# Kernel optimization log

Hardware: AMD Instinct MI355X
Metric: run time of the kernel (lower is better)

Reference implementation:

```python
import jax, jax.numpy as jnp
import numpy as np

I, H, V, T, B = 108, 1024, 108, 180, 512


def setup_inputs() -> dict:
    key = jax.random.key(0)
    ks = jax.random.split(key, 13)
    sc = 1.0 / np.sqrt(H).astype(np.float32)
    rn = lambda k, shape: (jax.random.normal(k, shape, jnp.float32) * sc)
    return {
        "x": jax.random.normal(ks[0], (T, B, I), jnp.float32),
        # LSTMCell 1 (input -> hidden)
        "W_ih1": rn(ks[1], (4 * H, I)), "W_hh1": rn(ks[2], (4 * H, H)),
        "b_ih1": rn(ks[3], (4 * H,)), "b_hh1": rn(ks[4], (4 * H,)),
        # mid Linear (hidden -> hidden)
        "W_mid": rn(ks[5], (H, H)), "b_mid": rn(ks[6], (H,)),
        # LSTMCell 2 (hidden -> hidden)
        "W_ih2": rn(ks[7], (4 * H, H)), "W_hh2": rn(ks[8], (4 * H, H)),
        "b_ih2": rn(ks[9], (4 * H,)), "b_hh2": rn(ks[10], (4 * H,)),
        # final Linear (hidden -> output)
        "W_fin": rn(ks[11], (V, H)), "b_fin": rn(ks[12], (V,)),
    }


def _lstm_cell(xt, h, c, W_ih, W_hh, b_ih, b_hh):
    # PyTorch LSTMCell gate order: input, forget, cell(g), output
    gates = xt @ W_ih.T + b_ih + h @ W_hh.T + b_hh  # [B, 4H]
    i, f, g, o = jnp.split(gates, 4, axis=-1)
    c_new = jax.nn.sigmoid(f) * c + jax.nn.sigmoid(i) * jnp.tanh(g)
    h_new = jax.nn.sigmoid(o) * jnp.tanh(c_new)
    return h_new, c_new


def reference(x, W_ih1, W_hh1, b_ih1, b_hh1, W_mid, b_mid,
              W_ih2, W_hh2, b_ih2, b_hh2, W_fin, b_fin):
    Bsz = x.shape[1]
    Hsz = W_hh1.shape[1]

    def step(carry, xt):
        h1, c1, h2, c2 = carry
        h1, c1 = _lstm_cell(xt, h1, c1, W_ih1, W_hh1, b_ih1, b_hh1)
        # NOTE: original feeds the CELL state (state1) into mid, not hidden1
        m = c1 @ W_mid.T + b_mid
        h2, c2 = _lstm_cell(m, h2, c2, W_ih2, W_hh2, b_ih2, b_hh2)
        # final also reads the cell state (state2); dropout is identity (eval)
        out = jax.nn.log_softmax(c2 @ W_fin.T + b_fin, axis=-1)
        return (h1, c1, h2, c2), out

    init = tuple(jnp.zeros((Bsz, Hsz), x.dtype) for _ in range(4))
    (h1, c1, h2, c2), outs = jax.lax.scan(step, init, x)  # outs: [T, B, V]
    return outs
```

## Files before the change

### kernel.cpp

```cpp
#include <hip/hip_runtime.h>
#include <stdint.h>


typedef unsigned short u16;
typedef __attribute__((ext_vector_type(2))) float f32x2;
typedef __attribute__((ext_vector_type(4))) float f32x4;
typedef __attribute__((ext_vector_type(8))) short bf16x8;
typedef unsigned long long u64;

#define HDIM 1024
#define BSZ  512
#define TSTEPS 180
#define IIN  108
#define VOUT 108
#define NBLK 256

#define AGENT __HIP_MEMORY_SCOPE_AGENT
#define RLX   __ATOMIC_RELAXED

__device__ __forceinline__ u16 f2bf(float x) {
  union { float f; unsigned u; } v; v.f = x;
  unsigned r = (v.u + 0x7fffu + ((v.u >> 16) & 1u)) >> 16;
  return (u16)r;
}
// ... 1 lines not shown
  union { unsigned u; float f; } v; v.u = (b & 0xffffu) << 16; return v.f;
}
__device__ __forceinline__ float sigm(float x) { return 1.f / (1.f + __expf(-x)); }
__device__ __forceinline__ float tanh_(float x) {
  float a = fabsf(x), t = __expf(-2.f * a);
  float r = (1.f - t) / (1.f + t);
  return x < 0.f ? -r : r;
}
__device__ __forceinline__ int permrow(int n) { return ((n & 1023) << 2) | (n >> 10); }

template <int AUX>
__device__ __forceinline__ void load16_lds(const void* g, void* l) {
  __builtin_amdgcn_global_load_lds(
      (const __attribute__((address_space(1))) unsigned int*)g,
      (__attribute__((address_space(3))) unsigned int*)l, 16, 0, AUX);
}

__device__ __forceinline__ void st32(void* p, unsigned v) {
  __hip_atomic_store((unsigned*)p, v, RLX, AGENT);
}
__device__ __forceinline__ void st64(void* p, u64 v) {
  __hip_atomic_store((u64*)p, v, RLX, AGENT);
}
__device__ __forceinline__ u64 ld64(const void* p) {
  return __hip_atomic_load((u64*)p, RLX, AGENT);
}

__device__ __forceinline__ void grid_sync(unsigned* bar, int grp) {
  __syncthreads();
  if (threadIdx.x == 0) {
    unsigned* gen  = bar;
    unsigned* root = bar + 32;
    unsigned* gcnt = bar + 64 + grp * 32;
    unsigned g = __hip_atomic_load(gen, RLX, AGENT);
    asm volatile("s_waitcnt vmcnt(0)" ::: "memory");
    unsigned a = __hip_atomic_fetch_add(gcnt, 1u, RLX, AGENT);
    if (a == 31u) {
      __hip_atomic_store(gcnt, 0u, RLX, AGENT);
      asm volatile("s_waitcnt vmcnt(0)" ::: "memory");
      unsigned c = __hip_atomic_fetch_add(root, 1u, RLX, AGENT);
      if (c == 7u) {
        __hip_atomic_store(root, 0u, RLX, AGENT);
        asm volatile("s_waitcnt vmcnt(0)" ::: "memory");
        __hip_atomic_store(gen, g + 1u, RLX, AGENT);
      }
    }
    while (__hip_atomic_load(gen, RLX, AGENT) == g)
      __builtin_amdgcn_s_sleep(2);
  }
  __syncthreads();
}

template <int AUXA>
__device__ __forceinline__ void stage128(const u16* A, const u16* B, int K,
                                         int k0, int m0, int n0,
                                         char* smem, int buf, int wave, int lane) {
  u16* As = (u16*)(smem + buf * 32768);
  u16* Bs = (u16*)(smem + buf * 32768 + 16384);
#pragma unroll
  for (int i = 0; i < 4; ++i) {
    int c = (wave * 4 + i) * 64 + lane;
    int row = c >> 3, lc = (c & 7) ^ (row & 7);
    const u16* g = A + (size_t)(m0 + row) * K + k0 + (lc << 3);
    load16_lds<AUXA>(g, As + c * 8);
  }
#pragma unroll
  for (int i = 0; i < 4; ++i) {
    int c = (wave * 4 + i) * 64 + lane;
    int row = c >> 3, lc = (c & 7) ^ (row & 7);
    const u16* g = B + (size_t)(n0 + row) * K + k0 + (lc << 3);
    load16_lds<0>(g, Bs + c * 8);
  }
}

__device__ __forceinline__ void compute128(f32x4 acc[4][4], char* smem, int buf,
                                           int wm, int wn, int l16, int quad) {
  const bf16x8* Av = (const bf16x8*)(smem + buf * 32768);
  const bf16x8* Bv = (const bf16x8*)(smem + buf * 32768 + 16384);
  const int sw = l16 & 7;
#pragma unroll
  for (int kk = 0; kk < 2; ++kk) {
    const int pc = (kk * 4 + quad) ^ sw;
    bf16x8 a[4], b[4];
#pragma unroll
    for (int mt = 0; mt < 4; ++mt)
      a[mt] = Av[(wm * 64 + mt * 16 + l16) * 8 + pc];
#pragma unroll
    for (int nt = 0; nt < 4; ++nt)
      b[nt] = Bv[(wn * 64 + nt * 16 + l16) * 8 + pc];
#pragma unroll
    for (int mt = 0; mt < 4; ++mt)
#pragma unroll
      for (int nt = 0; nt < 4; ++nt)
        acc[mt][nt] = __builtin_amdgcn_mfma_f32_16x16x32_bf16(
            a[mt], b[nt], acc[mt][nt], 0, 0, 0);
  }
}

template <bool HAS0>
__device__ __forceinline__ void gemm128(f32x4 acc[4][4],
    const u16* A0, const u16* B0, int K0,
    const u16* A1, const u16* B1, int K1,
    int m0, int n0, char* smem) {
  const int tid = threadIdx.x;
  const int lane = tid & 63, wave = tid >> 6;
  const int quad = lane >> 4, l16 = lane & 15;
  const int wm = wave >> 1, wn = wave & 1;

#pragma unroll
  for (int mt = 0; mt < 4; ++mt)
#pragma unroll
    for (int nt = 0; nt < 4; ++nt) {
      f32x4 z = {0.f, 0.f, 0.f, 0.f};
      acc[mt][nt] = z;
    }

  const int n0i = HAS0 ? (K0 >> 6) : 0;
  const int nIter = n0i + (K1 >> 6);

  auto do_stage = [&](int ix) {
    if (HAS0 && ix < n0i)
      stage128<0>(A0, B0, K0, ix * 64, m0, n0, smem, ix & 3, wave, lane);
    else
      stage128<0x11>(A1, B1, K1, (ix - n0i) * 64, m0, n0, smem, ix & 3, wave, lane);
  };

  do_stage(0);
  if (nIter > 1) do_stage(1);
  if (nIter > 2) do_stage(2);

  for (int it = 0; it < nIter; ++it) {
    if (it + 3 < nIter) do_stage(it + 3);
    const int rem = nIter - 1 - it;
    if (rem >= 3)      asm volatile("s_waitcnt vmcnt(24)" ::: "memory");
    else if (rem == 2) asm volatile("s_waitcnt vmcnt(16)" ::: "memory");
    else if (rem == 1) asm volatile("s_waitcnt vmcnt(8)"  ::: "memory");
    else               asm volatile("s_waitcnt vmcnt(0)"  ::: "memory");
    __builtin_amdgcn_s_barrier();
    asm volatile("" ::: "memory");
    compute128(acc, smem, it & 3, wm, wn, l16, quad);
    asm volatile("" ::: "memory");
    __builtin_amdgcn_s_barrier();
  }
}

__device__ __forceinline__ void stage_pb(const u16* A, const u16* B, int k0,
                                         int m0, int n0, char* smem, int buf,
                                         int wave, int lane) {
  u16* As = (u16*)(smem + buf * 24576);
  u16* Bs = (u16*)(smem + buf * 24576 + 16384);
#pragma unroll
  for (int i = 0; i < 4; ++i) {
    int c = (wave * 4 + i) * 64 + lane;
    int row = c >> 3, lc = (c & 7) ^ (row & 7);
    load16_lds<0x11>(A + (size_t)(m0 + row) * 1024 + k0 + (lc << 3), As + c * 8);
  }
#pragma unroll
  for (int i = 0; i < 2; ++i) {
    int c = (wave * 2 + i) * 64 + lane;
    int row = c >> 3, lc = (c & 7) ^ (row & 7);
    load16_lds<0>(B + (size_t)(n0 + row) * 1024 + k0 + (lc << 3), Bs + c * 8);
  }
}

__device__ __forceinline__ void compute_pb(f32x4 acc[4][2], char* smem, int buf,
                                           int wm, int wn, int l16, int quad) {
  const bf16x8* Av = (const bf16x8*)(smem + buf * 24576);
  const bf16x8* Bv = (const bf16x8*)(smem + buf * 24576 + 16384);
  const int sw = l16 & 7;
#pragma unroll
  for (int kk = 0; kk < 2; ++kk) {
    const int pc = (kk * 4 + quad) ^ sw;
    bf16x8 a[4], b[2];
#pragma unroll
    for (int mt = 0; mt < 4; ++mt)
      a[mt] = Av[(wm * 64 + mt * 16 + l16) * 8 + pc];
#pragma unroll
    for (int nt = 0; nt < 2; ++nt)
      b[nt] = Bv[(wn * 32 + nt * 16 + l16) * 8 + pc];
#pragma unroll
    for (int mt = 0; mt < 4; ++mt)
#pragma unroll
      for (int nt = 0; nt < 2; ++nt)
        acc[mt][nt] = __builtin_amdgcn_mfma_f32_16x16x32_bf16(
            a[mt], b[nt], acc[mt][nt], 0, 0, 0);
  }
}

__global__ __launch_bounds__(256, 1) void lstm_persistent(
    const u16* __restrict__ Xbf, const u16* __restrict__ W1a,
    const u16* __restrict__ Whh1b, const float* __restrict__ b1s,
    float* __restrict__ C1f, u16* __restrict__ C1b,
    const u16* __restrict__ Whh2b, const float* __restrict__ b2s,
    u16* __restrict__ U2, const u16* __restrict__ Wcombb,
    float* __restrict__ C2f, u16* __restrict__ C2seq,
    u16* __restrict__ H1x, u16* __restrict__ H1y,
    u16* __restrict__ H2x, u16* __restrict__ H2y,
    unsigned* __restrict__ bar)
{
  __shared__ __align__(16) char smem[131072];
  const int tid = threadIdx.x;
  const int lane = tid & 63, wave = tid >> 6;
  const int quad = lane >> 4, l16 = lane & 15;
  const int wm = wave >> 1, wn = wave & 1;
  const int b = blockIdx.x;
  const int grp = b & 7;

  for (int t = 0; t < TSTEPS; ++t) {
    const int p = t & 1;
    const u16* H1in = p ? H1y : H1x;  u16* H1o = p ? H1x : H1y;
    const u16* H2in = p ? H2y : H2x;  u16* H2o = p ? H2x : H2y;
    const u16* Xt = Xbf + (size_t)t * BSZ * 128;

    if (b < 128) {
      f32x4 acc[4][4];
      const int m0 = (b >> 5) * 128, n0 = (b & 31) * 128;
      gemm128<true>(acc, Xt, W1a, 128, H1in, Whh1b, 1024, m0, n0, smem);

      float* gl = (float*)smem;
      const int jbase = (b & 31) * 32;
#pragma unroll
      for (int h = 0; h < 2; ++h) {
        __syncthreads();
        if (wm == h) {
#pragma unroll
          for (int nt = 0; nt < 4; ++nt) {
            int col = wn * 64 + nt * 16 + l16;
#pragma unroll
            for (int mt = 0; mt < 4; ++mt) {
              int rowb = mt * 16 + quad * 4;
#pragma unroll
              for (int r = 0; r < 4; ++r)
                gl[(rowb + r) * 132 + col] = acc[mt][nt][r];
            }
          }
        }
        __syncthreads();
#pragma unroll
        for (int itr = 0; itr < 4; ++itr) {
          int idx = itr * 256 + tid;
          int mr = idx >> 4, jp = idx & 15;
          const float* gp = gl + mr * 132 + jp * 8;
          f32x4 ga = *(const f32x4*)gp;
          f32x4 gb = *(const f32x4*)(gp + 4);
          const float* bp = b1s + jbase * 4 + jp * 8;
          ga += *(const f32x4*)bp;
          gb += *(const f32x4*)(bp + 4);
          size_t off = (size_t)(m0 + h * 64 + mr) * HDIM + jbase + jp * 2;
          f32x2 cp = *(const f32x2*)(C1f + off);
          float c0 = sigm(ga[1]) * cp[0] + sigm(ga[0]) * tanh_(ga[2]);
          float c1 = sigm(gb[1]) * cp[1] + sigm(gb[0]) * tanh_(gb[2]);
          float h0 = sigm(ga[3]) * tanh_(c0);
          float h1 = sigm(gb[3]) * tanh_(c1);
          f32x2 cn = {c0, c1};
          *(f32x2*)(C1f + off) = cn;
          st32(H1o + off, (unsigned)f2bf(h0) | ((unsigned)f2bf(h1) << 16));
          st32(C1b + off, (unsigned)f2bf(c0) | ((unsigned)f2bf(c1) << 16));
        }
      }
    } else {
      f32x4 acc[4][4];
      const int bb = b - 128;
      const int m0 = (bb >> 5) * 128, n0 = (bb & 31) * 128;
      gemm128<false>(acc, nullptr, nullptr, 0, H2in, Whh2b, 1024, m0, n0, smem);
#pragma unroll
      for (int nt = 0; nt < 4; ++nt) {
        int col = n0 + wn * 64 + nt * 16 + l16;
        float bias = b2s[col];
#pragma unroll
        for (int mt = 0; mt < 4; ++mt) {
          int row = m0 + wm * 64 + mt * 16 + quad * 4;
#pragma unroll
          for (int r = 0; r < 4; ++r) {
            float v = acc[mt][nt][r] + bias;
            float w = __shfl_xor(v, 1);
            if (!(lane & 1))
              st32(U2 + (size_t)(row + r) * 4096 + col,
                   (unsigned)f2bf(v) | ((unsigned)f2bf(w) << 16));
          }
        }
      }
    }
    grid_sync(bar, grp);

    {
      f32x4 acc[4][2];
#pragma unroll
      for (int mt = 0; mt < 4; ++mt)
#pragma unroll
        for (int nt = 0; nt < 2; ++nt) {
          f32x4 z = {0.f, 0.f, 0.f, 0.f};
          acc[mt][nt] = z;
        }
      const int m0 = (b >> 6) * 128;
      const int n0 = (b & 63) * 64;
      const int jbase = (b & 63) * 16;

      stage_pb(C1b, Wcombb, 0,   m0, n0, smem, 0, wave, lane);
      stage_pb(C1b, Wcombb, 64,  m0, n0, smem, 1, wave, lane);
      stage_pb(C1b, Wcombb, 128, m0, n0, smem, 2, wave, lane);
      for (int it = 0; it < 16; ++it) {
        if (it + 3 < 16)
          stage_pb(C1b, Wcombb, (it + 3) * 64, m0, n0, smem, (it + 3) & 3, wave, lane);
        const int rem = 15 - it;
        if (rem >= 3)      asm volatile("s_waitcnt vmcnt(18)" ::: "memory");
        else if (rem == 2) asm volatile("s_waitcnt vmcnt(12)" ::: "memory");
        else if (rem == 1) asm volatile("s_waitcnt vmcnt(6)"  ::: "memory");
        else               asm volatile("s_waitcnt vmcnt(0)"  ::: "memory");
        __builtin_amdgcn_s_barrier();
        asm volatile("" ::: "memory");
        compute_pb(acc, smem, it & 3, wm, wn, l16, quad);
        asm volatile("" ::: "memory");
        __builtin_amdgcn_s_barrier();
      }

      float* gl = (float*)smem;
      __syncthreads();
#pragma unroll
      for (int nt = 0; nt < 2; ++nt) {
        int col = wn * 32 + nt * 16 + l16;
#pragma unroll
        for (int mt = 0; mt < 4; ++mt) {
          int rowb = wm * 64 + mt * 16 + quad * 4;
#pragma unroll
          for (int r = 0; r < 4; ++r)
            gl[(rowb + r) * 68 + col] = acc[mt][nt][r];
        }
      }
      __syncthreads();
      u16* C2dst = C2seq + (size_t)t * BSZ * HDIM;
#pragma unroll
      for (int itr = 0; itr < 4; ++itr) {
        int idx = itr * 256 + tid;
        int mr = idx >> 3, jp = idx & 7;
        int grow = m0 + mr;
        const float* gp = gl + mr * 68 + jp * 8;
        f32x4 ga = *(const f32x4*)gp;
        f32x4 gb = *(const f32x4*)(gp + 4);
        const u16* u2p = U2 + (size_t)grow * 4096 + (jbase + jp * 2) * 4;
        u64 ua = ld64(u2p);
        u64 ub = ld64(u2p + 4);
        ga[0] += bf2f((unsigned)ua);        ga[1] += bf2f((unsigned)(ua >> 16));
        ga[2] += bf2f((unsigned)(ua >> 32)); ga[3] += bf2f((unsigned)(ua >> 48));
        gb[0] += bf2f((unsigned)ub);        gb[1] += bf2f((unsigned)(ub >> 16));
        gb[2] += bf2f((unsigned)(ub >> 32)); gb[3] += bf2f((unsigned)(ub >> 48));
        size_t off = (size_t)grow * HDIM + jbase + jp * 2;
        union { u64 u; float f[2]; } cv;
        cv.u = ld64(C2f + off);
        float c0 = sigm(ga[1]) * cv.f[0] + sigm(ga[0]) * tanh_(ga[2]);
        float c1 = sigm(gb[1]) * cv.f[1] + sigm(gb[0]) * tanh_(gb[2]);
        float h0 = sigm(ga[3]) * tanh_(c0);
        float h1 = sigm(gb[3]) * tanh_(c1);
        cv.f[0] = c0; cv.f[1] = c1;
        st64(C2f + off, cv.u);
        st32(H2o + off, (unsigned)f2bf(h0) | ((unsigned)f2bf(h1) << 16));
        st32(C2dst + off, (unsigned)f2bf(c0) | ((unsigned)f2bf(c1) << 16));
      }
    }
    grid_sync(bar, grp);
  }
}

__global__ __launch_bounds__(256, 1) void k1_fused(
    const u16* __restrict__ Xt, const u16* __restrict__ W1a,
    const u16* __restrict__ H1in, const u16* __restrict__ Whh1,
    const float* __restrict__ b1s, float* __restrict__ c1State,
    u16* __restrict__ H1out, u16* __restrict__ C1out,
    const u16* __restrict__ H2in, const u16* __restrict__ Whh2,
    const float* __restrict__ b2s, u16* __restrict__ U2)
{
  __shared__ __align__(16) char smem[131072];
  const int tid = threadIdx.x;
  const int lane = tid & 63, wave = tid >> 6;
  const int quad = lane >> 4, l16 = lane & 15;
  const int wm = wave >> 1, wn = wave & 1;
  const int b = blockIdx.x;
  f32x4 acc[4][4];

  if (b < 128) {
    const int m0 = (b >> 5) * 128, n0 = (b & 31) * 128;
    gemm128<true>(acc, Xt, W1a, 128, H1in, Whh1, 1024, m0, n0, smem);

    float* gl = (float*)smem;
    const int jbase = (b & 31) * 32;
#pragma unroll
    for (int h = 0; h < 2; ++h) {
      __syncthreads();
      if (wm == h) {
#pragma unroll
        for (int nt = 0; nt < 4; ++nt) {
          int col = wn * 64 + nt * 16 + l16;
#pragma unroll
          for (int mt = 0; mt < 4; ++mt) {
            int rowb = mt * 16 + quad * 4;
#pragma unroll
            for (int r = 0; r < 4; ++r)
              gl[(rowb + r) * 132 + col] = acc[mt][nt][r];
          }
        }
      }
      __syncthreads();
#pragma unroll
      for (int itr = 0; itr < 8; ++itr) {
        int idx = itr * 256 + tid;
        int mr = idx >> 5, jl = idx & 31;
        f32x4 g4 = *(const f32x4*)(gl + mr * 132 + jl * 4);
        f32x4 b4 = *(const f32x4*)(b1s + jbase * 4 + jl * 4);
        g4 += b4;
        float ii = sigm(g4[0]), ff = sigm(g4[1]);
        float gg = tanh_(g4[2]), oo = sigm(g4[3]);
        size_t off = (size_t)(m0 + h * 64 + mr) * HDIM + jbase + jl;
        float cp = c1State[off];
        float cn = ff * cp + ii * gg;
        float hh = oo * tanh_(cn);
        c1State[off] = cn;
// ... 294 lines not shown
  const size_t SZ_C2S = (size_t)TSTEPS * BSZ * HDIM * 2;

  char* base = (char*)d_ws;
  size_t off = 0;
  auto alloc = [&](size_t b) { char* p = base + off; off += (b + 255) & ~(size_t)255; return p; };

  u16*   Xbf    = (u16*)alloc(SZ_XBF);
  u16*   W1a    = (u16*)alloc(SZ_W1A);
  u16*   Whh1b  = (u16*)alloc(SZ_W1K);
  u16*   Wcombb = (u16*)alloc(SZ_W1K);
  u16*   Whh2b  = (u16*)alloc(SZ_W1K);
  u16*   Wih2b  = (u16*)alloc(SZ_W1K);
  u16*   WmidT  = (u16*)alloc(SZ_WMT);
  u16*   Wfinb  = (u16*)alloc(SZ_WFB);
  float* b1s    = (float*)alloc(SZ_BSM);
  float* b2s    = (float*)alloc(SZ_BSM);
  u16*   H1p[2]; H1p[0] = (u16*)alloc(SZ_HB); H1p[1] = (u16*)alloc(SZ_HB);
  u16*   H2p[2]; H2p[0] = (u16*)alloc(SZ_HB); H2p[1] = (u16*)alloc(SZ_HB);
  float* C1f    = (float*)alloc(SZ_CF);
  float* C2f    = (float*)alloc(SZ_CF);
  u16*   C1b    = (u16*)alloc(SZ_HB);
  u16*   C2b    = (u16*)alloc(SZ_HB);
  u16*   U2     = (u16*)alloc(SZ_U2);
  unsigned* barp = (unsigned*)alloc(2048);
  u16*   C2seq  = (u16*)(base + off);
  bool batched  = (off + SZ_C2S) <= ws_size;

  size_t zbytes = 4 * SZ_HB + 2 * SZ_CF;
  hipMemsetAsync((void*)H1p[0], 0, zbytes, stream);
  hipMemsetAsync((void*)barp, 0, 2048, stream);

  k_build_w1a<<<2048, 256, 0, stream>>>(Wih1, W1a);
  k_conv_perm1024<<<16384, 256, 0, stream>>>(Whh1, Whh1b);
  k_conv_perm1024<<<16384, 256, 0, stream>>>(Whh2, Whh2b);
  k_conv<<<16384, 256, 0, stream>>>(Wih2, Wih2b);
  k_transpose1024<<<4096, 256, 0, stream>>>(Wmid, WmidT);
  k_build_wfin<<<512, 256, 0, stream>>>(Wfin, Wfinb);
  k_build_xpad<<<46080, 256, 0, stream>>>(x, Xbf);
  k_b1sum<<<16, 256, 0, stream>>>(bih1, bhh1, b1s);
  k_b2sum<<<1024, 256, 0, stream>>>(Wih2, bmid, bih2, bhh2, b2s);
  wcomb_gemm<<<dim3(8, 64), 256, 0, stream>>>(Wih2b, WmidT, Wcombb);

  bool usedPersistent = false;
  if (batched) {
    u16* H1x = H1p[0]; u16* H1y = H1p[1];
    u16* H2x = H2p[0]; u16* H2y = H2p[1];
    void* kargs[] = {
        (void*)&Xbf, (void*)&W1a, (void*)&Whh1b, (void*)&b1s,
        (void*)&C1f, (void*)&C1b, (void*)&Whh2b, (void*)&b2s,
        (void*)&U2, (void*)&Wcombb, (void*)&C2f, (void*)&C2seq,
        (void*)&H1x, (void*)&H1y, (void*)&H2x, (void*)&H2y,
        (void*)&barp};
    hipError_t ce = hipLaunchCooperativeKernel(
        (const void*)lstm_persistent, dim3(NBLK), dim3(256), kargs, 0, stream);
    usedPersistent = (ce == hipSuccess);
    if (!usedPersistent) (void)hipGetLastError();
  }

  if (usedPersistent) {
    final_logsoftmax<<<dim3(1, (TSTEPS * BSZ) / 64), 256, 0, stream>>>(
        C2seq, Wfinb, bfin, (float*)d_out);
  } else {
    for (int t = 0; t < TSTEPS; ++t) {
      int p = t & 1;
      k1_fused<<<256, 256, 0, stream>>>(
          Xbf + (size_t)t * BSZ * 128, W1a, H1p[p], Whh1b, b1s, C1f,
          H1p[p ^ 1], C1b, H2p[p], Whh2b, b2s, U2);
      u16* c2dst = batched ? (C2seq + (size_t)t * BSZ * HDIM) : C2b;
      k2_cell2<<<128, 256, 0, stream>>>(C1b, Wcombb, U2, C2f, H2p[p ^ 1], c2dst);
      if (!batched)
        final_logsoftmax<<<dim3(1, 8), 256, 0, stream>>>(
            C2b, Wfinb, bfin, (float*)d_out + (size_t)t * BSZ * VOUT);
    }
    if (batched)
      final_logsoftmax<<<dim3(1, (TSTEPS * BSZ) / 64), 256, 0, stream>>>(
          C2seq, Wfinb, bfin, (float*)d_out);
  }
}
```

Before: 6.854 ms.

## Use 8 waves per block in persistent LSTM kernel

After: 5.753 ms, median of 2. 1.19x faster.

```diff
diff --git a/kernel.cpp b/kernel.cpp
--- a/kernel.cpp
+++ b/kernel.cpp
@@ -77,65 +77,63 @@
 }
 
 template <int AUXA>
-__device__ __forceinline__ void stage128(const u16* A, const u16* B, int K,
-                                         int k0, int m0, int n0,
-                                         char* smem, int buf, int wave, int lane) {
+__device__ __forceinline__ void stage128_8w(const u16* A, const u16* B, int K,
+                                            int k0, int m0, int n0,
+                                            char* smem, int buf, int wave, int lane) {
   u16* As = (u16*)(smem + buf * 32768);
   u16* Bs = (u16*)(smem + buf * 32768 + 16384);
 #pragma unroll
-  for (int i = 0; i < 4; ++i) {
-    int c = (wave * 4 + i) * 64 + lane;
+  for (int i = 0; i < 2; ++i) {
+    int c = (wave * 2 + i) * 64 + lane;
     int row = c >> 3, lc = (c & 7) ^ (row & 7);
-    const u16* g = A + (size_t)(m0 + row) * K + k0 + (lc << 3);
-    load16_lds<AUXA>(g, As + c * 8);
-  }
-#pragma unroll
-  for (int i = 0; i < 4; ++i) {
-    int c = (wave * 4 + i) * 64 + lane;
+    load16_lds<AUXA>(A + (size_t)(m0 + row) * K + k0 + (lc << 3), As + c * 8);
+  }
+#pragma unroll
+  for (int i = 0; i < 2; ++i) {
+    int c = (wave * 2 + i) * 64 + lane;
     int row = c >> 3, lc = (c & 7) ^ (row & 7);
-    const u16* g = B + (size_t)(n0 + row) * K + k0 + (lc << 3);
-    load16_lds<0>(g, Bs + c * 8);
-  }
-}
-
-__device__ __forceinline__ void compute128(f32x4 acc[4][4], char* smem, int buf,
-                                           int wm, int wn, int l16, int quad) {
+    load16_lds<0>(B + (size_t)(n0 + row) * K + k0 + (lc << 3), Bs + c * 8);
+  }
+}
+
+__device__ __forceinline__ void compute128_8w(f32x4 acc[4][2], char* smem, int buf,
+                                              int wm, int wn, int l16, int quad) {
   const bf16x8* Av = (const bf16x8*)(smem + buf * 32768);
   const bf16x8* Bv = (const bf16x8*)(smem + buf * 32768 + 16384);
   const int sw = l16 & 7;
 #pragma unroll
   for (int kk = 0; kk < 2; ++kk) {
     const int pc = (kk * 4 + quad) ^ sw;
-    bf16x8 a[4], b[4];
+    bf16x8 a[4], b[2];
 #pragma unroll
     for (int mt = 0; mt < 4; ++mt)
       a[mt] = Av[(wm * 64 + mt * 16 + l16) * 8 + pc];
 #pragma unroll
-    for (int nt = 0; nt < 4; ++nt)
-      b[nt] = Bv[(wn * 64 + nt * 16 + l16) * 8 + pc];
+    for (int nt = 0; nt < 2; ++nt)
+      b[nt] = Bv[(wn * 32 + nt * 16 + l16) * 8 + pc];
 #pragma unroll
     for (int mt = 0; mt < 4; ++mt)
 #pragma unroll
-      for (int nt = 0; nt < 4; ++nt)
+      for (int nt = 0; nt < 2; ++nt)
         acc[mt][nt] = __builtin_amdgcn_mfma_f32_16x16x32_bf16(
             a[mt], b[nt], acc[mt][nt], 0, 0, 0);
   }
 }
 
 template <bool HAS0>
-__device__ __forceinline__ void gemm128(f32x4 acc[4][4],
+__device__ __forceinline__ void gemm128_8w(f32x4 acc[4][2],
     const u16* A0, const u16* B0, int K0,
     const u16* A1, const u16* B1, int K1,
     int m0, int n0, char* smem) {
   const int tid = threadIdx.x;
   const int lane = tid & 63, wave = tid >> 6;
   const int quad = lane >> 4, l16 = lane & 15;
-  const int wm = wave >> 1, wn = wave & 1;
+  const int wm = wave >> 2, wn = wave & 3;
 
 #pragma unroll
   for (int mt = 0; mt < 4; ++mt)
 #pragma unroll
-    for (int nt = 0; nt < 4; ++nt) {
+    for (int nt = 0; nt < 2; ++nt) {
       f32x4 z = {0.f, 0.f, 0.f, 0.f};
       acc[mt][nt] = z;
     }
@@ -145,9 +143,9 @@
 
   auto do_stage = [&](int ix) {
     if (HAS0 && ix < n0i)
-      stage128<0>(A0, B0, K0, ix * 64, m0, n0, smem, ix & 3, wave, lane);
+      stage128_8w<0>(A0, B0, K0, ix * 64, m0, n0, smem, ix & 3, wave, lane);
     else
-      stage128<0x11>(A1, B1, K1, (ix - n0i) * 64, m0, n0, smem, ix & 3, wave, lane);
+      stage128_8w<0x11>(A1, B1, K1, (ix - n0i) * 64, m0, n0, smem, ix & 3, wave, lane);
   };
 
   do_stage(0);
@@ -157,62 +155,56 @@
   for (int it = 0; it < nIter; ++it) {
     if (it + 3 < nIter) do_stage(it + 3);
     const int rem = nIter - 1 - it;
-    if (rem >= 3)      asm volatile("s_waitcnt vmcnt(24)" ::: "memory");
-    else if (rem == 2) asm volatile("s_waitcnt vmcnt(16)" ::: "memory");
-    else if (rem == 1) asm volatile("s_waitcnt vmcnt(8)"  ::: "memory");
+    if (rem >= 3)      asm volatile("s_waitcnt vmcnt(12)" ::: "memory");
+    else if (rem == 2) asm volatile("s_waitcnt vmcnt(8)"  ::: "memory");
+    else if (rem == 1) asm volatile("s_waitcnt vmcnt(4)"  ::: "memory");
     else               asm volatile("s_waitcnt vmcnt(0)"  ::: "memory");
     __builtin_amdgcn_s_barrier();
     asm volatile("" ::: "memory");
-    compute128(acc, smem, it & 3, wm, wn, l16, quad);
+    compute128_8w(acc, smem, it & 3, wm, wn, l16, quad);
     asm volatile("" ::: "memory");
     __builtin_amdgcn_s_barrier();
   }
 }
 
-__device__ __forceinline__ void stage_pb(const u16* A, const u16* B, int k0,
-                                         int m0, int n0, char* smem, int buf,
-                                         int wave, int lane) {
+__device__ __forceinline__ void stage_pb_8w(const u16* A, const u16* B, int k0,
+                                            int m0, int n0, char* smem, int buf,
+                                            int wave, int lane) {
   u16* As = (u16*)(smem + buf * 24576);
   u16* Bs = (u16*)(smem + buf * 24576 + 16384);
-#pragma unroll
-  for (int i = 0; i < 4; ++i) {
-    int c = (wave * 4 + i) * 64 + lane;
-    int row = c >> 3, lc = (c & 7) ^ (row & 7);
-    load16_lds<0x11>(A + (size_t)(m0 + row) * 1024 + k0 + (lc << 3), As + c * 8);
-  }
 #pragma unroll
   for (int i = 0; i < 2; ++i) {
     int c = (wave * 2 + i) * 64 + lane;
     int row = c >> 3, lc = (c & 7) ^ (row & 7);
+    load16_lds<0x11>(A + (size_t)(m0 + row) * 1024 + k0 + (lc << 3), As + c * 8);
+  }
+  {
+    int c = wave * 64 + lane;
+    int row = c >> 3, lc = (c & 7) ^ (row & 7);
     load16_lds<0>(B + (size_t)(n0 + row) * 1024 + k0 + (lc << 3), Bs + c * 8);
   }
 }
 
-__device__ __forceinline__ void compute_pb(f32x4 acc[4][2], char* smem, int buf,
-                                           int wm, int wn, int l16, int quad) {
+__device__ __forceinline__ void compute_pb_8w(f32x4 acc[4], char* smem, int buf,
+                                              int wm, int wn, int l16, int quad) {
   const bf16x8* Av = (const bf16x8*)(smem + buf * 24576);
   const bf16x8* Bv = (const bf16x8*)(smem + buf * 24576 + 16384);
   const int sw = l16 & 7;
 #pragma unroll
   for (int kk = 0; kk < 2; ++kk) {
     const int pc = (kk * 4 + quad) ^ sw;
-    bf16x8 a[4], b[2];
+    bf16x8 a[4], b;
 #pragma unroll
     for (int mt = 0; mt < 4; ++mt)
       a[mt] = Av[(wm * 64 + mt * 16 + l16) * 8 + pc];
-#pragma unroll
-    for (int nt = 0; nt < 2; ++nt)
-      b[nt] = Bv[(wn * 32 + nt * 16 + l16) * 8 + pc];
+    b = Bv[(wn * 16 + l16) * 8 + pc];
 #pragma unroll
     for (int mt = 0; mt < 4; ++mt)
-#pragma unroll
-      for (int nt = 0; nt < 2; ++nt)
-        acc[mt][nt] = __builtin_amdgcn_mfma_f32_16x16x32_bf16(
-            a[mt], b[nt], acc[mt][nt], 0, 0, 0);
-  }
-}
-
-__global__ __launch_bounds__(256, 1) void lstm_persistent(
+      acc[mt] = __builtin_amdgcn_mfma_f32_16x16x32_bf16(a[mt], b, acc[mt], 0, 0, 0);
+  }
+}
+
+__global__ __launch_bounds__(512, 1) void lstm_persistent(
     const u16* __restrict__ Xbf, const u16* __restrict__ W1a,
     const u16* __restrict__ Whh1b, const float* __restrict__ b1s,
     float* __restrict__ C1f, u16* __restrict__ C1b,
@@ -227,7 +219,7 @@
   const int tid = threadIdx.x;
   const int lane = tid & 63, wave = tid >> 6;
   const int quad = lane >> 4, l16 = lane & 15;
-  const int wm = wave >> 1, wn = wave & 1;
+  const int wm = wave >> 2, wn = wave & 3;
   const int b = blockIdx.x;
   const int grp = b & 7;
 
@@ -238,9 +230,9 @@
     const u16* Xt = Xbf + (size_t)t * BSZ * 128;
 
     if (b < 128) {
-      f32x4 acc[4][4];
+      f32x4 acc[4][2];
       const int m0 = (b >> 5) * 128, n0 = (b & 31) * 128;
-      gemm128<true>(acc, Xt, W1a, 128, H1in, Whh1b, 1024, m0, n0, smem);
+      gemm128_8w<true>(acc, Xt, W1a, 128, H1in, Whh1b, 1024, m0, n0, smem);
 
       float* gl = (float*)smem;
       const int jbase = (b & 31) * 32;
@@ -249,8 +241,8 @@
         __syncthreads();
         if (wm == h) {
 #pragma unroll
-          for (int nt = 0; nt < 4; ++nt) {
-            int col = wn * 64 + nt * 16 + l16;
+          for (int nt = 0; nt < 2; ++nt) {
+            int col = wn * 32 + nt * 16 + l16;
 #pragma unroll
             for (int mt = 0; mt < 4; ++mt) {
               int rowb = mt * 16 + quad * 4;
@@ -262,8 +254,8 @@
         }
         __syncthreads();
 #pragma unroll
-        for (int itr = 0; itr < 4; ++itr) {
-          int idx = itr * 256 + tid;
+        for (int itr = 0; itr < 2; ++itr) {
+          int idx = itr * 512 + tid;
           int mr = idx >> 4, jp = idx & 15;
           const float* gp = gl + mr * 132 + jp * 8;
           f32x4 ga = *(const f32x4*)gp;
@@ -284,13 +276,13 @@
         }
       }
     } else {
-      f32x4 acc[4][4];
+      f32x4 acc[4][2];
       const int bb = b - 128;
       const int m0 = (bb >> 5) * 128, n0 = (bb & 31) * 128;
-      gemm128<false>(acc, nullptr, nullptr, 0, H2in, Whh2b, 1024, m0, n0, smem);
-#pragma unroll
-      for (int nt = 0; nt < 4; ++nt) {
-        int col = n0 + wn * 64 + nt * 16 + l16;
+      gemm128_8w<false>(acc, nullptr, nullptr, 0, H2in, Whh2b, 1024, m0, n0, smem);
+#pragma unroll
+      for (int nt = 0; nt < 2; ++nt) {
+        int col = n0 + wn * 32 + nt * 16 + l16;
         float bias = b2s[col];
 #pragma unroll
         for (int mt = 0; mt < 4; ++mt) {
@@ -309,54 +301,51 @@
     grid_sync(bar, grp);
 
     {
-      f32x4 acc[4][2];
-#pragma unroll
-      for (int mt = 0; mt < 4; ++mt)
-#pragma unroll
-        for (int nt = 0; nt < 2; ++nt) {
-          f32x4 z = {0.f, 0.f, 0.f, 0.f};
-          acc[mt][nt] = z;
-        }
+      f32x4 acc[4];
+#pragma unroll
+      for (int mt = 0; mt < 4; ++mt) {
+        f32x4 z = {0.f, 0.f, 0.f, 0.f};
+        acc[mt] = z;
+      }
       const int m0 = (b >> 6) * 128;
       const int n0 = (b & 63) * 64;
       const int jbase = (b & 63) * 16;
 
-      stage_pb(C1b, Wcombb, 0,   m0, n0, smem, 0, wave, lane);
-      stage_pb(C1b, Wcombb, 64,  m0, n0, smem, 1, wave, lane);
-      stage_pb(C1b, Wcombb, 128, m0, n0, smem, 2, wave, lane);
+      stage_pb_8w(C1b, Wcombb, 0,   m0, n0, smem, 0, wave, lane);
+      stage_pb_8w(C1b, Wcombb, 64,  m0, n0, smem, 1, wave, lane);
+      stage_pb_8w(C1b, Wcombb, 128, m0, n0, smem, 2, wave, lane);
       for (int it = 0; it < 16; ++it) {
         if (it + 3 < 16)
-          stage_pb(C1b, Wcombb, (it + 3) * 64, m0, n0, smem, (it + 3) & 3, wave, lane);
+          stage_pb_8w(C1b, Wcombb, (it + 3) * 64, m0, n0, smem, (it + 3) & 3, wave, lane);
         const int rem = 15 - it;
-        if (rem >= 3)      asm volatile("s_waitcnt vmcnt(18)" ::: "memory");
-        else if (rem == 2) asm volatile("s_waitcnt vmcnt(12)" ::: "memory");
-        else if (rem == 1) asm volatile("s_waitcnt vmcnt(6)"  ::: "memory");
-        else               asm volatile("s_waitcnt vmcnt(0)"  ::: "memory");
+        if (rem >= 3)      asm volatile("s_waitcnt vmcnt(9)" ::: "memory");
+        else if (rem == 2) asm volatile("s_waitcnt vmcnt(6)" ::: "memory");
+        else if (rem == 1) asm volatile("s_waitcnt vmcnt(3)" ::: "memory");
+        else               asm volatile("s_waitcnt vmcnt(0)" ::: "memory");
         __builtin_amdgcn_s_barrier();
         asm volatile("" ::: "memory");
-        compute_pb(acc, smem, it & 3, wm, wn, l16, quad);
+        compute_pb_8w(acc, smem, it & 3, wm, wn, l16, quad);
         asm volatile("" ::: "memory");
         __builtin_amdgcn_s_barrier();
       }
 
       float* gl = (float*)smem;
       __syncthreads();
-#pragma unroll
-      for (int nt = 0; nt < 2; ++nt) {
-        int col = wn * 32 + nt * 16 + l16;
+      {
+        int col = wn * 16 + l16;
 #pragma unroll
         for (int mt = 0; mt < 4; ++mt) {
           int rowb = wm * 64 + mt * 16 + quad * 4;
 #pragma unroll
           for (int r = 0; r < 4; ++r)
-            gl[(rowb + r) * 68 + col] = acc[mt][nt][r];
+            gl[(rowb + r) * 68 + col] = acc[mt][r];
         }
       }
       __syncthreads();
       u16* C2dst = C2seq + (size_t)t * BSZ * HDIM;
 #pragma unroll
-      for (int itr = 0; itr < 4; ++itr) {
-        int idx = itr * 256 + tid;
+      for (int itr = 0; itr < 2; ++itr) {
+        int idx = itr * 512 + tid;
         int mr = idx >> 3, jp = idx & 7;
         int grow = m0 + mr;
         const float* gp = gl + mr * 68 + jp * 8;
@@ -386,6 +375,97 @@
   }
 }
 
+template <int AUXA>
+__device__ __forceinline__ void stage128(const u16* A, const u16* B, int K,
+                                         int k0, int m0, int n0,
+                                         char* smem, int buf, int wave, int lane) {
+  u16* As = (u16*)(smem + buf * 32768);
+  u16* Bs = (u16*)(smem + buf * 32768 + 16384);
+#pragma unroll
+  for (int i = 0; i < 4; ++i) {
+    int c = (wave * 4 + i) * 64 + lane;
+    int row = c >> 3, lc = (c & 7) ^ (row & 7);
+    load16_lds<AUXA>(A + (size_t)(m0 + row) * K + k0 + (lc << 3), As + c * 8);
+  }
+#pragma unroll
+  for (int i = 0; i < 4; ++i) {
+    int c = (wave * 4 + i) * 64 + lane;
+    int row = c >> 3, lc = (c & 7) ^ (row & 7);
+    load16_lds<0>(B + (size_t)(n0 + row) * K + k0 + (lc << 3), Bs + c * 8);
+  }
+}
+
+__device__ __forceinline__ void compute128(f32x4 acc[4][4], char* smem, int buf,
+                                           int wm, int wn, int l16, int quad) {
+  const bf16x8* Av = (const bf16x8*)(smem + buf * 32768);
+  const bf16x8* Bv = (const bf16x8*)(smem + buf * 32768 + 16384);
+  const int sw = l16 & 7;
+#pragma unroll
+  for (int kk = 0; kk < 2; ++kk) {
+    const int pc = (kk * 4 + quad) ^ sw;
+    bf16x8 a[4], b[4];
+#pragma unroll
+    for (int mt = 0; mt < 4; ++mt)
+      a[mt] = Av[(wm * 64 + mt * 16 + l16) * 8 + pc];
+#pragma unroll
+    for (int nt = 0; nt < 4; ++nt)
+      b[nt] = Bv[(wn * 64 + nt * 16 + l16) * 8 + pc];
+#pragma unroll
+    for (int mt = 0; mt < 4; ++mt)
+#pragma unroll
+      for (int nt = 0; nt < 4; ++nt)
+        acc[mt][nt] = __builtin_amdgcn_mfma_f32_16x16x32_bf16(
+            a[mt], b[nt], acc[mt][nt], 0, 0, 0);
+  }
+}
+
+template <bool HAS0>
+__device__ __forceinline__ void gemm128(f32x4 acc[4][4],
+    const u16* A0, const u16* B0, int K0,
+    const u16* A1, const u16* B1, int K1,
+    int m0, int n0, char* smem) {
+  const int tid = threadIdx.x;
+  const int lane = tid & 63, wave = tid >> 6;
+  const int quad = lane >> 4, l16 = lane & 15;
+  const int wm = wave >> 1, wn = wave & 1;
+
+#pragma unroll
+  for (int mt = 0; mt < 4; ++mt)
+#pragma unroll
+    for (int nt = 0; nt < 4; ++nt) {
+      f32x4 z = {0.f, 0.f, 0.f, 0.f};
+      acc[mt][nt] = z;
+    }
+
+  const int n0i = HAS0 ? (K0 >> 6) : 0;
+  const int nIter = n0i + (K1 >> 6);
+
+  auto do_stage = [&](int ix) {
+    if (HAS0 && ix < n0i)
+      stage128<0>(A0, B0, K0, ix * 64, m0, n0, smem, ix & 3, wave, lane);
+    else
+      stage128<0x11>(A1, B1, K1, (ix - n0i) * 64, m0, n0, smem, ix & 3, wave, lane);
+  };
+
+  do_stage(0);
+  if (nIter > 1) do_stage(1);
+  if (nIter > 2) do_stage(2);
+
+  for (int it = 0; it < nIter; ++it) {
+    if (it + 3 < nIter) do_stage(it + 3);
+    const int rem = nIter - 1 - it;
+    if (rem >= 3)      asm volatile("s_waitcnt vmcnt(24)" ::: "memory");
+    else if (rem == 2) asm volatile("s_waitcnt vmcnt(16)" ::: "memory");
+    else if (rem == 1) asm volatile("s_waitcnt vmcnt(8)"  ::: "memory");
+    else               asm volatile("s_waitcnt vmcnt(0)"  ::: "memory");
+    __builtin_amdgcn_s_barrier();
+    asm volatile("" ::: "memory");
+    compute128(acc, smem, it & 3, wm, wn, l16, quad);
+    asm volatile("" ::: "memory");
+    __builtin_amdgcn_s_barrier();
+  }
+}
+
 __global__ __launch_bounds__(256, 1) void k1_fused(
     const u16* __restrict__ Xt, const u16* __restrict__ W1a,
     const u16* __restrict__ H1in, const u16* __restrict__ Whh1,
@@ -786,7 +866,7 @@
         (void*)&H1x, (void*)&H1y, (void*)&H2x, (void*)&H2y,
         (void*)&barp};
     hipError_t ce = hipLaunchCooperativeKernel(
-        (const void*)lstm_persistent, dim3(NBLK), dim3(256), kargs, 0, stream);
+        (const void*)lstm_persistent, dim3(NBLK), dim3(512), kargs, 0, stream);
     usedPersistent = (ce == hipSuccess);
     if (!usedPersistent) (void)hipGetLastError();
   }
```

## Use 8 waves per block with split-K across wave pairs in persistent LSTM

Applied to the files above, without the earlier changes.

Measured after the change: 8.697 ms. 26.9% more time.

```diff
diff --git a/kernel.cpp b/kernel.cpp
--- a/kernel.cpp
+++ b/kernel.cpp
@@ -77,42 +77,40 @@
 }
 
 template <int AUXA>
-__device__ __forceinline__ void stage128(const u16* A, const u16* B, int K,
-                                         int k0, int m0, int n0,
-                                         char* smem, int buf, int wave, int lane) {
-  u16* As = (u16*)(smem + buf * 32768);
-  u16* Bs = (u16*)(smem + buf * 32768 + 16384);
+__device__ __forceinline__ void stageA(const u16* A, const u16* B, int lda, int ldb,
+                                       int k0, int m0, int n0,
+                                       char* smem, int buf, int wave, int lane) {
+  u16* As = (u16*)(smem + buf * 65536);
+  u16* Bs = (u16*)(smem + buf * 65536 + 32768);
 #pragma unroll
   for (int i = 0; i < 4; ++i) {
     int c = (wave * 4 + i) * 64 + lane;
-    int row = c >> 3, lc = (c & 7) ^ (row & 7);
-    const u16* g = A + (size_t)(m0 + row) * K + k0 + (lc << 3);
-    load16_lds<AUXA>(g, As + c * 8);
+    int row = c >> 4, lc = (c & 15) ^ (row & 15);
+    load16_lds<AUXA>(A + (size_t)(m0 + row) * lda + k0 + (lc << 3), As + c * 8);
   }
 #pragma unroll
   for (int i = 0; i < 4; ++i) {
     int c = (wave * 4 + i) * 64 + lane;
-    int row = c >> 3, lc = (c & 7) ^ (row & 7);
-    const u16* g = B + (size_t)(n0 + row) * K + k0 + (lc << 3);
-    load16_lds<0>(g, Bs + c * 8);
-  }
-}
-
-__device__ __forceinline__ void compute128(f32x4 acc[4][4], char* smem, int buf,
-                                           int wm, int wn, int l16, int quad) {
-  const bf16x8* Av = (const bf16x8*)(smem + buf * 32768);
-  const bf16x8* Bv = (const bf16x8*)(smem + buf * 32768 + 16384);
-  const int sw = l16 & 7;
-#pragma unroll
-  for (int kk = 0; kk < 2; ++kk) {
-    const int pc = (kk * 4 + quad) ^ sw;
+    int row = c >> 4, lc = (c & 15) ^ (row & 15);
+    load16_lds<0>(B + (size_t)(n0 + row) * ldb + k0 + (lc << 3), Bs + c * 8);
+  }
+}
+
+__device__ __forceinline__ void computeA(f32x4 acc[4][4], char* smem, int buf,
+                                         int qm, int qn, int kh, int l16, int quad) {
+  const bf16x8* Av = (const bf16x8*)(smem + buf * 65536);
+  const bf16x8* Bv = (const bf16x8*)(smem + buf * 65536 + 32768);
+#pragma unroll
+  for (int kk2 = 0; kk2 < 2; ++kk2) {
+    const int lchunk = (kh * 2 + kk2) * 4 + quad;
+    const int pc = lchunk ^ l16;
     bf16x8 a[4], b[4];
 #pragma unroll
     for (int mt = 0; mt < 4; ++mt)
-      a[mt] = Av[(wm * 64 + mt * 16 + l16) * 8 + pc];
+      a[mt] = Av[(qm * 64 + mt * 16 + l16) * 16 + pc];
 #pragma unroll
     for (int nt = 0; nt < 4; ++nt)
-      b[nt] = Bv[(wn * 64 + nt * 16 + l16) * 8 + pc];
+      b[nt] = Bv[(qn * 64 + nt * 16 + l16) * 16 + pc];
 #pragma unroll
     for (int mt = 0; mt < 4; ++mt)
 #pragma unroll
@@ -123,15 +121,11 @@
 }
 
 template <bool HAS0>
-__device__ __forceinline__ void gemm128(f32x4 acc[4][4],
-    const u16* A0, const u16* B0, int K0,
-    const u16* A1, const u16* B1, int K1,
-    int m0, int n0, char* smem) {
-  const int tid = threadIdx.x;
-  const int lane = tid & 63, wave = tid >> 6;
-  const int quad = lane >> 4, l16 = lane & 15;
-  const int wm = wave >> 1, wn = wave & 1;
-
+__device__ __forceinline__ void gemmA(f32x4 acc[4][4],
+    const u16* A0, const u16* B0,
+    const u16* A1, const u16* B1,
+    int m0, int n0, char* smem,
+    int wave, int lane, int qm, int qn, int kh, int l16, int quad) {
 #pragma unroll
   for (int mt = 0; mt < 4; ++mt)
 #pragma unroll
@@ -139,70 +133,66 @@
       f32x4 z = {0.f, 0.f, 0.f, 0.f};
       acc[mt][nt] = z;
     }
-
-  const int n0i = HAS0 ? (K0 >> 6) : 0;
-  const int nIter = n0i + (K1 >> 6);
+  const int n0i = HAS0 ? 1 : 0;
+  const int nIter = n0i + 8;
 
   auto do_stage = [&](int ix) {
-    if (HAS0 && ix < n0i)
-      stage128<0>(A0, B0, K0, ix * 64, m0, n0, smem, ix & 3, wave, lane);
+    if (HAS0 && ix == 0)
+      stageA<0>(A0, B0, 128, 128, 0, m0, n0, smem, ix & 1, wave, lane);
     else
-      stage128<0x11>(A1, B1, K1, (ix - n0i) * 64, m0, n0, smem, ix & 3, wave, lane);
+      stageA<0x11>(A1, B1, 1024, 1024, (ix - n0i) * 128, m0, n0, smem, ix & 1, wave, lane);
   };
 
   do_stage(0);
-  if (nIter > 1) do_stage(1);
-  if (nIter > 2) do_stage(2);
-
   for (int it = 0; it < nIter; ++it) {
-    if (it + 3 < nIter) do_stage(it + 3);
-    const int rem = nIter - 1 - it;
-    if (rem >= 3)      asm volatile("s_waitcnt vmcnt(24)" ::: "memory");
-    else if (rem == 2) asm volatile("s_waitcnt vmcnt(16)" ::: "memory");
-    else if (rem == 1) asm volatile("s_waitcnt vmcnt(8)"  ::: "memory");
-    else               asm volatile("s_waitcnt vmcnt(0)"  ::: "memory");
+    if (it + 1 < nIter) {
+      do_stage(it + 1);
+      asm volatile("s_waitcnt vmcnt(8)" ::: "memory");
+    } else {
+      asm volatile("s_waitcnt vmcnt(0)" ::: "memory");
+    }
     __builtin_amdgcn_s_barrier();
     asm volatile("" ::: "memory");
-    compute128(acc, smem, it & 3, wm, wn, l16, quad);
+    computeA(acc, smem, it & 1, qm, qn, kh, l16, quad);
     asm volatile("" ::: "memory");
     __builtin_amdgcn_s_barrier();
   }
 }
 
-__device__ __forceinline__ void stage_pb(const u16* A, const u16* B, int k0,
-                                         int m0, int n0, char* smem, int buf,
-                                         int wave, int lane) {
-  u16* As = (u16*)(smem + buf * 24576);
-  u16* Bs = (u16*)(smem + buf * 24576 + 16384);
+__device__ __forceinline__ void stageB(const u16* A, const u16* B, int k0,
+                                       int m0, int n0, char* smem, int buf,
+                                       int wave, int lane) {
+  u16* As = (u16*)(smem + buf * 49152);
+  u16* Bs = (u16*)(smem + buf * 49152 + 32768);
 #pragma unroll
   for (int i = 0; i < 4; ++i) {
     int c = (wave * 4 + i) * 64 + lane;
-    int row = c >> 3, lc = (c & 7) ^ (row & 7);
+    int row = c >> 4, lc = (c & 15) ^ (row & 15);
     load16_lds<0x11>(A + (size_t)(m0 + row) * 1024 + k0 + (lc << 3), As + c * 8);
   }
 #pragma unroll
   for (int i = 0; i < 2; ++i) {
     int c = (wave * 2 + i) * 64 + lane;
-    int row = c >> 3, lc = (c & 7) ^ (row & 7);
+    int row = c >> 4, lc = (c & 15) ^ (row & 15);
     load16_lds<0>(B + (size_t)(n0 + row) * 1024 + k0 + (lc << 3), Bs + c * 8);
   }
 }
 
-__device__ __forceinline__ void compute_pb(f32x4 acc[4][2], char* smem, int buf,
-                                           int wm, int wn, int l16, int quad) {
-  const bf16x8* Av = (const bf16x8*)(smem + buf * 24576);
-  const bf16x8* Bv = (const bf16x8*)(smem + buf * 24576 + 16384);
-  const int sw = l16 & 7;
-#pragma unroll
-  for (int kk = 0; kk < 2; ++kk) {
-    const int pc = (kk * 4 + quad) ^ sw;
+__device__ __forceinline__ void computeB(f32x4 acc[4][2], char* smem, int buf,
+                                         int qm, int qn, int kh, int l16, int quad) {
+  const bf16x8* Av = (const bf16x8*)(smem + buf * 49152);
+  const bf16x8* Bv = (const bf16x8*)(smem + buf * 49152 + 32768);
+#pragma unroll
+  for (int kk2 = 0; kk2 < 2; ++kk2) {
+    const int lchunk = (kh * 2 + kk2) * 4 + quad;
+    const int pc = lchunk ^ l16;
     bf16x8 a[4], b[2];
 #pragma unroll
     for (int mt = 0; mt < 4; ++mt)
-      a[mt] = Av[(wm * 64 + mt * 16 + l16) * 8 + pc];
+      a[mt] = Av[(qm * 64 + mt * 16 + l16) * 16 + pc];
 #pragma unroll
     for (int nt = 0; nt < 2; ++nt)
-      b[nt] = Bv[(wn * 32 + nt * 16 + l16) * 8 + pc];
+      b[nt] = Bv[(qn * 32 + nt * 16 + l16) * 16 + pc];
 #pragma unroll
     for (int mt = 0; mt < 4; ++mt)
 #pragma unroll
@@ -212,7 +202,7 @@
   }
 }
 
-__global__ __launch_bounds__(256, 1) void lstm_persistent(
+__global__ __launch_bounds__(512, 1) void lstm_persistent(
     const u16* __restrict__ Xbf, const u16* __restrict__ W1a,
     const u16* __restrict__ Whh1b, const float* __restrict__ b1s,
     float* __restrict__ C1f, u16* __restrict__ C1b,
@@ -227,7 +217,7 @@
   const int tid = threadIdx.x;
   const int lane = tid & 63, wave = tid >> 6;
   const int quad = lane >> 4, l16 = lane & 15;
-  const int wm = wave >> 1, wn = wave & 1;
+  const int qm = wave >> 2, qn = (wave >> 1) & 1, kh = wave & 1;
   const int b = blockIdx.x;
   const int grp = b & 7;
 
@@ -240,17 +230,18 @@
     if (b < 128) {
       f32x4 acc[4][4];
       const int m0 = (b >> 5) * 128, n0 = (b & 31) * 128;
-      gemm128<true>(acc, Xt, W1a, 128, H1in, Whh1b, 1024, m0, n0, smem);
+      gemmA<true>(acc, Xt, W1a, H1in, Whh1b, m0, n0, smem,
+                  wave, lane, qm, qn, kh, l16, quad);
 
       float* gl = (float*)smem;
       const int jbase = (b & 31) * 32;
 #pragma unroll
       for (int h = 0; h < 2; ++h) {
         __syncthreads();
-        if (wm == h) {
+        if (qm == h && kh == 1) {
 #pragma unroll
           for (int nt = 0; nt < 4; ++nt) {
-            int col = wn * 64 + nt * 16 + l16;
+            int col = qn * 64 + nt * 16 + l16;
 #pragma unroll
             for (int mt = 0; mt < 4; ++mt) {
               int rowb = mt * 16 + quad * 4;
@@ -261,9 +252,23 @@
           }
         }
         __syncthreads();
-#pragma unroll
-        for (int itr = 0; itr < 4; ++itr) {
-          int idx = itr * 256 + tid;
+        if (qm == h && kh == 0) {
+#pragma unroll
+          for (int nt = 0; nt < 4; ++nt) {
+            int col = qn * 64 + nt * 16 + l16;
+#pragma unroll
+            for (int mt = 0; mt < 4; ++mt) {
+              int rowb = mt * 16 + quad * 4;
+#pragma unroll
+              for (int r = 0; r < 4; ++r)
+                gl[(rowb + r) * 132 + col] += acc[mt][nt][r];
+            }
+          }
+        }
+        __syncthreads();
+#pragma unroll
+        for (int itr = 0; itr < 2; ++itr) {
+          int idx = itr * 512 + tid;
           int mr = idx >> 4, jp = idx & 15;
           const float* gp = gl + mr * 132 + jp * 8;
           f32x4 ga = *(const f32x4*)gp;
@@ -287,23 +292,47 @@
       f32x4 acc[4][4];
       const int bb = b - 128;
       const int m0 = (bb >> 5) * 128, n0 = (bb & 31) * 128;
-      gemm128<false>(acc, nullptr, nullptr, 0, H2in, Whh2b, 1024, m0, n0, smem);
-#pragma unroll
-      for (int nt = 0; nt < 4; ++nt) {
-        int col = n0 + wn * 64 + nt * 16 + l16;
-        float bias = b2s[col];
-#pragma unroll
-        for (int mt = 0; mt < 4; ++mt) {
-          int row = m0 + wm * 64 + mt * 16 + quad * 4;
-#pragma unroll
-          for (int r = 0; r < 4; ++r) {
-            float v = acc[mt][nt][r] + bias;
-            float w = __shfl_xor(v, 1);
-            if (!(lane & 1))
-              st32(U2 + (size_t)(row + r) * 4096 + col,
-                   (unsigned)f2bf(v) | ((unsigned)f2bf(w) << 16));
+      gemmA<false>(acc, nullptr, nullptr, H2in, Whh2b, m0, n0, smem,
+                   wave, lane, qm, qn, kh, l16, quad);
+      float* gl = (float*)smem;
+      __syncthreads();
+      if (kh == 1) {
+#pragma unroll
+        for (int nt = 0; nt < 4; ++nt) {
+          int col = qn * 64 + nt * 16 + l16;
+#pragma unroll
+          for (int mt = 0; mt < 4; ++mt) {
+            int rowb = qm * 64 + mt * 16 + quad * 4;
+#pragma unroll
+            for (int r = 0; r < 4; ++r)
+              gl[(rowb + r) * 132 + col] = acc[mt][nt][r];
           }
         }
+      }
+      __syncthreads();
+      if (kh == 0) {
+#pragma unroll
+        for (int nt = 0; nt < 4; ++nt) {
+          int col = qn * 64 + nt * 16 + l16;
+#pragma unroll
+          for (int mt = 0; mt < 4; ++mt) {
+            int rowb = qm * 64 + mt * 16 + quad * 4;
+#pragma unroll
+            for (int r = 0; r < 4; ++r)
+              gl[(rowb + r) * 132 + col] += acc[mt][nt][r];
+          }
+        }
+      }
+      __syncthreads();
+#pragma unroll
+      for (int itr = 0; itr < 16; ++itr) {
+        int idx = itr * 512 + tid;
+        int mr = idx >> 6, jp = idx & 63;
+        int col = n0 + jp * 2;
+        float v0 = gl[mr * 132 + jp * 2]     + b2s[col];
+        float v1 = gl[mr * 132 + jp * 2 + 1] + b2s[col + 1];
+        st32(U2 + (size_t)(m0 + mr) * 4096 + col,
+             (unsigned)f2bf(v0) | ((unsigned)f2bf(v1) << 16));
       }
     }
     grid_sync(bar, grp);
@@ -321,42 +350,55 @@
       const int n0 = (b & 63) * 64;
       const int jbase = (b & 63) * 16;
 
-      stage_pb(C1b, Wcombb, 0,   m0, n0, smem, 0, wave, lane);
-      stage_pb(C1b, Wcombb, 64,  m0, n0, smem, 1, wave, lane);
-      stage_pb(C1b, Wcombb, 128, m0, n0, smem, 2, wave, lane);
-      for (int it = 0; it < 16; ++it) {
-        if (it + 3 < 16)
-          stage_pb(C1b, Wcombb, (it + 3) * 64, m0, n0, smem, (it + 3) & 3, wave, lane);
-        const int rem = 15 - it;
-        if (rem >= 3)      asm volatile("s_waitcnt vmcnt(18)" ::: "memory");
-        else if (rem == 2) asm volatile("s_waitcnt vmcnt(12)" ::: "memory");
-        else if (rem == 1) asm volatile("s_waitcnt vmcnt(6)"  ::: "memory");
-        else               asm volatile("s_waitcnt vmcnt(0)"  ::: "memory");
+      stageB(C1b, Wcombb, 0, m0, n0, smem, 0, wave, lane);
+      for (int it = 0; it < 8; ++it) {
+        if (it + 1 < 8) {
+          stageB(C1b, Wcombb, (it + 1) * 128, m0, n0, smem, (it + 1) & 1, wave, lane);
+          asm volatile("s_waitcnt vmcnt(6)" ::: "memory");
+        } else {
+          asm volatile("s_waitcnt vmcnt(0)" ::: "memory");
+        }
         __builtin_amdgcn_s_barrier();
         asm volatile("" ::: "memory");
-        compute_pb(acc, smem, it & 3, wm, wn, l16, quad);
+        computeB(acc, smem, it & 1, qm, qn, kh, l16, quad);
         asm volatile("" ::: "memory");
         __builtin_amdgcn_s_barrier();
       }
 
       float* gl = (float*)smem;
       __syncthreads();
-#pragma unroll
-      for (int nt = 0; nt < 2; ++nt) {
-        int col = wn * 32 + nt * 16 + l16;
-#pragma unroll
-        for (int mt = 0; mt < 4; ++mt) {
-          int rowb = wm * 64 + mt * 16 + quad * 4;
-#pragma unroll
-          for (int r = 0; r < 4; ++r)
-            gl[(rowb + r) * 68 + col] = acc[mt][nt][r];
+      if (kh == 1) {
+#pragma unroll
+        for (int nt = 0; nt < 2; ++nt) {
+          int col = qn * 32 + nt * 16 + l16;
+#pragma unroll
+          for (int mt = 0; mt < 4; ++mt) {
+            int rowb = qm * 64 + mt * 16 + quad * 4;
+#pragma unroll
+            for (int r = 0; r < 4; ++r)
+              gl[(rowb + r) * 68 + col] = acc[mt][nt][r];
+          }
+        }
+      }
+      __syncthreads();
+      if (kh == 0) {
+#pragma unroll
+        for (int nt = 0; nt < 2; ++nt) {
+          int col = qn * 32 + nt * 16 + l16;
+#pragma unroll
+          for (int mt = 0; mt < 4; ++mt) {
+            int rowb = qm * 64 + mt * 16 + quad * 4;
+#pragma unroll
+            for (int r = 0; r < 4; ++r)
+              gl[(rowb + r) * 68 + col] += acc[mt][nt][r];
+          }
         }
       }
       __syncthreads();
       u16* C2dst = C2seq + (size_t)t * BSZ * HDIM;
 #pragma unroll
-      for (int itr = 0; itr < 4; ++itr) {
-        int idx = itr * 256 + tid;
+      for (int itr = 0; itr < 2; ++itr) {
+        int idx = itr * 512 + tid;
         int mr = idx >> 3, jp = idx & 7;
         int grow = m0 + mr;
         const float* gp = gl + mr * 68 + jp * 8;
@@ -386,6 +428,97 @@
   }
 }
 
+template <int AUXA>
+__device__ __forceinline__ void stage128(const u16* A, const u16* B, int K,
+                                         int k0, int m0, int n0,
+                                         char* smem, int buf, int wave, int lane) {
+  u16* As = (u16*)(smem + buf * 32768);
+  u16* Bs = (u16*)(smem + buf * 32768 + 16384);
+#pragma unroll
+  for (int i = 0; i < 4; ++i) {
+    int c = (wave * 4 + i) * 64 + lane;
+    int row = c >> 3, lc = (c & 7) ^ (row & 7);
+    load16_lds<AUXA>(A + (size_t)(m0 + row) * K + k0 + (lc << 3), As + c * 8);
+  }
+#pragma unroll
+  for (int i = 0; i < 4; ++i) {
+    int c = (wave * 4 + i) * 64 + lane;
+    int row = c >> 3, lc = (c & 7) ^ (row & 7);
+    load16_lds<0>(B + (size_t)(n0 + row) * K + k0 + (lc << 3), Bs + c * 8);
+  }
+}
+
+__device__ __forceinline__ void compute128(f32x4 acc[4][4], char* smem, int buf,
+                                           int wm, int wn, int l16, int quad) {
+  const bf16x8* Av = (const bf16x8*)(smem + buf * 32768);
+  const bf16x8* Bv = (const bf16x8*)(smem + buf * 32768 + 16384);
+  const int sw = l16 & 7;
+#pragma unroll
+  for (int kk = 0; kk < 2; ++kk) {
+    const int pc = (kk * 4 + quad) ^ sw;
+    bf16x8 a[4], b[4];
+#pragma unroll
+    for (int mt = 0; mt < 4; ++mt)
+      a[mt] = Av[(wm * 64 + mt * 16 + l16) * 8 + pc];
+#pragma unroll
+    for (int nt = 0; nt < 4; ++nt)
+      b[nt] = Bv[(wn * 64 + nt * 16 + l16) * 8 + pc];
+#pragma unroll
+    for (int mt = 0; mt < 4; ++mt)
+#pragma unroll
+      for (int nt = 0; nt < 4; ++nt)
+        acc[mt][nt] = __builtin_amdgcn_mfma_f32_16x16x32_bf16(
+            a[mt], b[nt], acc[mt][nt], 0, 0, 0);
+  }
+}
+
+template <bool HAS0>
+__device__ __forceinline__ void gemm128(f32x4 acc[4][4],
+    const u16* A0, const u16* B0, int K0,
+    const u16* A1, const u16* B1, int K1,
+    int m0, int n0, char* smem) {
+  const int tid = threadIdx.x;
+  const int lane = tid & 63, wave = tid >> 6;
+  const int quad = lane >> 4, l16 = lane & 15;
+  const int wm = wave >> 1, wn = wave & 1;
+
+#pragma unroll
+  for (int mt = 0; mt < 4; ++mt)
+#pragma unroll
+    for (int nt = 0; nt < 4; ++nt) {
+      f32x4 z = {0.f, 0.f, 0.f, 0.f};
+      acc[mt][nt] = z;
+    }
+
+  const int n0i = HAS0 ? (K0 >> 6) : 0;
+  const int nIter = n0i + (K1 >> 6);
+
+  auto do_stage = [&](int ix) {
+    if (HAS0 && ix < n0i)
+      stage128<0>(A0, B0, K0, ix * 64, m0, n0, smem, ix & 3, wave, lane);
+    else
+      stage128<0x11>(A1, B1, K1, (ix - n0i) * 64, m0, n0, smem, ix & 3, wave, lane);
+  };
+
+  do_stage(0);
+  if (nIter > 1) do_stage(1);
+  if (nIter > 2) do_stage(2);
+
+  for (int it = 0; it < nIter; ++it) {
+    if (it + 3 < nIter) do_stage(it + 3);
+    const int rem = nIter - 1 - it;
+    if (rem >= 3)      asm volatile("s_waitcnt vmcnt(24)" ::: "memory");
+    else if (rem == 2) asm volatile("s_waitcnt vmcnt(16)" ::: "memory");
+    else if (rem == 1) asm volatile("s_waitcnt vmcnt(8)"  ::: "memory");
+    else               asm volatile("s_waitcnt vmcnt(0)"  ::: "memory");
+    __builtin_amdgcn_s_barrier();
+    asm volatile("" ::: "memory");
+    compute128(acc, smem, it & 3, wm, wn, l16, quad);
+    asm volatile("" ::: "memory");
+    __builtin_amdgcn_s_barrier();
+  }
+}
+
 __global__ __launch_bounds__(256, 1) void k1_fused(
     const u16* __restrict__ Xt, const u16* __restrict__ W1a,
     const u16* __restrict__ H1in, const u16* __restrict__ Whh1,
@@ -786,7 +919,7 @@
         (void*)&H1x, (void*)&H1y, (void*)&H2x, (void*)&H2y,
         (void*)&barp};
     hipError_t ce = hipLaunchCooperativeKernel(
-        (const void*)lstm_persistent, dim3(NBLK), dim3(256), kargs, 0, stream);
+        (const void*)lstm_persistent, dim3(NBLK), dim3(512), kargs, 0, stream);
     usedPersistent = (ce == hipSuccess);
     if (!usedPersistent) (void)hipGetLastError();
   }
```
